# Kernel tuning notes

Hardware: AMD Instinct MI355X
Metric: run time of the kernel (lower is better)

The kernel has to match this reference:

```python
import jax, jax.numpy as jnp
import numpy as np

B, S, D = 32, 256, 128
K = 16          # num_sample (negatives + the positive appended last)
V = 50000       # vocab / num_classes


def setup_inputs() -> dict:
    key = jax.random.key(0)
    k1, k2, k3, k4 = jax.random.split(key, 4)
    return {
        "input_latent": jax.random.normal(k1, (B, S, D), dtype=jnp.float32),
        "target_labels": jax.random.randint(k2, (B, S), 0, V, dtype=jnp.int64),
        "batch_samples": jax.random.randint(k3, (B, S * (K - 1)), 0, V, dtype=jnp.int64),
        "embed_weight": jax.random.normal(k4, (V, D), dtype=jnp.float32),
    }


def reference(input_latent, target_labels, batch_samples, embed_weight):
    b, s, d = input_latent.shape
    out_emb = embed_weight[target_labels]                      # [B,S,D] positives
    neg_emb = embed_weight[batch_samples].reshape(b, s, K - 1, d)
    # Candidates per target position j: K-1 negatives + the positive itself (last)
    samples = jnp.concatenate([neg_emb, out_emb[:, :, None, :]], axis=2)  # [B,S,K,D]
    # sample_rep[b,i,j,k] = latent[b,i] . samples[b,j,k]
    sample_scores = jnp.einsum('bid,bjkd->bijk', input_latent, samples)   # [B,S,S,K]
    # output_rep[b,i,j] = latent[b,i] . out_emb[b,j] (== sample_scores[...,K-1])
    out_scores = jnp.einsum('bid,bjd->bij', input_latent, out_emb)        # [B,S,S]
    # log( exp(out - max) / sum_k exp(sample - max) ) = out - logsumexp(sample)
    lse = jax.scipy.special.logsumexp(sample_scores, axis=3)              # [B,S,S]
    return out_scores - lse
```

## Files before the change

kernel.cpp:

```cpp
#include <hip/hip_runtime.h>
#include <hip/hip_bf16.h>
#include <math.h>

#define BB 32
#define SS 256
#define DD 128
#define KK 16
#define VV 50000
#define SK (SS*KK)
#define LOG2E 1.44269504f
#define LN2   0.69314718f

typedef __attribute__((ext_vector_type(8))) short bf16x8;
typedef __attribute__((ext_vector_type(4))) float f32x4;
typedef __attribute__((ext_vector_type(16))) float f32x16;
typedef unsigned short ushort_t;

static __device__ __forceinline__ short f2bf(float f) {
    __hip_bfloat16 h = __float2bfloat16(f);
    return *(short*)&h;
}

static __device__ __forceinline__ float fast_exp2(float x) {
    float r; asm("v_exp_f32 %0, %1" : "=v"(r) : "v"(x)); return r;
}
static __device__ __forceinline__ float fast_log2(float x) {
    float r; asm("v_log_f32 %0, %1" : "=v"(r) : "v"(x)); return r;
}

static __device__ __forceinline__ int lds_off(int row, int d) {
    return row * 256 + ((d * 2) ^ ((row & 15) << 4));
}

static __device__ __forceinline__ void gload_lds16(const void* g, void* lds) {
    __builtin_amdgcn_global_load_lds(
        (const __attribute__((address_space(1))) unsigned int*)g,
        (__attribute__((address_space(3))) unsigned int*)lds, 16, 0, 0);
}

#define NLAT (BB*SS*DD)
#define NCHUNK_LAT (NLAT/8)

__global__ __launch_bounds__(256)
void convert_lat_kernel(const float* __restrict__ latent,
                        ushort_t* __restrict__ ws_lat)
{
    int i = blockIdx.x * 256 + threadIdx.x;
    if (i >= NCHUNK_LAT) return;
    const float* src = latent + (size_t)i * 8;
    float f[8];
    *(f32x4*)(f + 0) = ((const f32x4*)src)[0];
    *(f32x4*)(f + 4) = ((const f32x4*)src)[1];
    short o[8];
    #pragma unroll
    for (int e = 0; e < 8; ++e) o[e] = f2bf(f[e] * LOG2E);
    *(bf16x8*)(ws_lat + (size_t)i * 8) = *(bf16x8*)o;
}

__global__ __launch_bounds__(256, 2)
void neg_loss_persist(const ushort_t* __restrict__ lat_bf,
                      const int*   __restrict__ labels,
                      const int*   __restrict__ samples,
                      const float* __restrict__ embed,
                      float* __restrict__ out)
{
    __shared__ char  ldsA[SS * 256];
    __shared__ float trans[256][9];

    const int p     = blockIdx.x;
    const int b     = p >> 4;
    const int npair = p & 15;
    const int tid   = threadIdx.x;
    const int wave  = tid >> 6;
    const int lane  = tid & 63;
    const int q     = lane & 15;
    const int sub   = lane >> 4;
    const int l31   = lane & 31;
    const int hi    = lane >> 5;

    const int rB  = wave * 32 + l31;
    const int gc0 = (npair * 2) * 128 + rB;
    const int gc1 = gc0 + 128;
    const int j0i = gc0 >> 4, k0i = gc0 & 15;
    const int j1i = gc1 >> 4, k1i = gc1 & 15;
    const int idx0 = (k0i < 15)
        ? samples[(size_t)b * (SS * (KK - 1)) + j0i * (KK - 1) + k0i]
        : labels[b * SS + j0i];
    const int idx1 = (k1i < 15)
        ? samples[(size_t)b * (SS * (KK - 1)) + j1i * (KK - 1) + k1i]
        : labels[b * SS + j1i];

    f32x4 fbA[16];
    {
        const float* rowp = embed + (size_t)idx0 * DD + hi * 8;
        #pragma unroll
        for (int ks = 0; ks < 8; ++ks) {
            fbA[2 * ks]     = *(const f32x4*)(rowp + ks * 16);
            fbA[2 * ks + 1] = *(const f32x4*)(rowp + ks * 16 + 4);
        }
    }

    #pragma unroll
    for (int t = 0; t < 16; ++t) {
        const int r0 = wave * 64 + t * 4;
        const int r  = r0 + sub;
        const ushort_t* src = lat_bf + ((size_t)(b * SS + r) * DD)
                                     + ((q ^ (r & 15)) << 3);
        gload_lds16(src, ldsA + r0 * 256);
    }

    __syncthreads();

    f32x4 fbB[16];
    {
        const float* rowp = embed + (size_t)idx1 * DD + hi * 8;
        #pragma unroll
        for (int ks = 0; ks < 8; ++ks) {
            fbB[2 * ks]     = *(const f32x4*)(rowp + ks * 16);
            fbB[2 * ks + 1] = *(const f32x4*)(rowp + ks * 16 + 4);
        }
    }

    #pragma unroll
    for (int t = 0; t < 2; ++t) {
        const int tile_n = npair * 2 + t;
        const int jc     = wave * 2 + hi;

        bf16x8 av[8];
        #pragma unroll
        for (int ks = 0; ks < 8; ++ks) {
            const f32x4 lo  = t ? fbB[2 * ks]     : fbA[2 * ks];
            const f32x4 hi4 = t ? fbB[2 * ks + 1] : fbA[2 * ks + 1];
            short t8[8];
            #pragma unroll
            for (int e = 0; e < 4; ++e) t8[e]     = f2bf(lo[e]);
            #pragma unroll
            for (int e = 0; e < 4; ++e) t8[4 + e] = f2bf(hi4[e]);
            av[ks] = *(bf16x8*)t8;
        }

        f32x16 acc[4][2] = {};
        #pragma unroll
        for (int ks = 0; ks < 8; ++ks) {
            const int d = ks * 16 + hi * 8;
            #pragma unroll
            for (int mt = 0; mt < 4; ++mt) {
                bf16x8 bv0 = *(const bf16x8*)(ldsA + lds_off(mt * 64 + l31, d));
                bf16x8 bv1 = *(const bf16x8*)(ldsA + lds_off(mt * 64 + 32 + l31, d));
                acc[mt][0] = __builtin_amdgcn_mfma_f32_32x32x16_bf16(av[ks], bv0, acc[mt][0], 0, 0, 0);
                acc[mt][1] = __builtin_amdgcn_mfma_f32_32x32x16_bf16(av[ks], bv1, acc[mt][1], 0, 0, 0);
            }
        }

        #pragma unroll
        for (int mt = 0; mt < 4; ++mt) {
            #pragma unroll
            for (int f = 0; f < 2; ++f) {
                const f32x16 v = acc[mt][f];
                float pm0 = fmaxf(fmaxf(fmaxf(v[0], v[1]), fmaxf(v[2], v[3])),
                                  fmaxf(fmaxf(v[4], v[5]), fmaxf(v[6], v[7])));
                float pm1 = fmaxf(fmaxf(fmaxf(v[8], v[9]), fmaxf(v[10], v[11])),
                                  fmaxf(fmaxf(v[12], v[13]), fmaxf(v[14], v[15])));
                float om0 = fmaxf(pm0, __shfl_xor(pm0, 32));
                float om1 = fmaxf(pm1, __shfl_xor(pm1, 32));
                float e0 = ((fast_exp2(v[0] - om0) + fast_exp2(v[1] - om0))
                          + (fast_exp2(v[2] - om0) + fast_exp2(v[3] - om0)))
                         + ((fast_exp2(v[4] - om0) + fast_exp2(v[5] - om0))
                          + (fast_exp2(v[6] - om0) + fast_exp2(v[7] - om0)));
                float e1 = ((fast_exp2(v[8]  - om1) + fast_exp2(v[9]  - om1))
                          + (fast_exp2(v[10] - om1) + fast_exp2(v[11] - om1)))
                         + ((fast_exp2(v[12] - om1) + fast_exp2(v[13] - om1))
                          + (fast_exp2(v[14] - om1) + fast_exp2(v[15] - om1)));
                float s0 = e0 + __shfl_xor(e0, 32);
                float s1 = e1 + __shfl_xor(e1, 32);
                float pos0 = __shfl_xor(v[7], 32);
                float pos1 = v[15];
                const float pos = hi ? pos1 : pos0;
                const float om  = hi ? om1  : om0;
                const float s   = hi ? s1   : s0;
                const int i = mt * 64 + f * 32 + l31;
                trans[i][jc] = (pos - om - fast_log2(s)) * LN2;
            }
        }

        __syncthreads();

        {
            const int i = tid;
            float r[8];
            #pragma unroll
            for (int c = 0; c < 8; ++c) r[c] = trans[i][c];
            float* dst = out + ((size_t)b * SS + i) * SS + tile_n * 8;
            *(f32x4*)(dst)     = *(f32x4*)(r);
            *(f32x4*)(dst + 4) = *(f32x4*)(r + 4);
        }

        if (t == 0) __syncthreads();
    }
}

__global__ __launch_bounds__(256, 2)
void neg_loss_fused(const float* __restrict__ latent,
                    const int*   __restrict__ labels,
                    const int*   __restrict__ samples,
                    const float* __restrict__ embed,
                    float* __restrict__ out)
{
    __shared__ char  ldsA[SS * 256];
    __shared__ float trans[256][9];

    const int p     = blockIdx.x;
    const int b     = p >> 4;
    const int npair = p & 15;
    const int tid   = threadIdx.x;
    const int wave  = tid >> 6;
    const int lane  = tid & 63;
    const int l31   = lane & 31;
    const int hi    = lane >> 5;

    const int rB  = wave * 32 + l31;
    const int gc0 = (npair * 2) * 128 + rB;
    const int gc1 = gc0 + 128;
    const int j0i = gc0 >> 4, k0i = gc0 & 15;
    const int j1i = gc1 >> 4, k1i = gc1 & 15;
    const int idx0 = (k0i < 15)
        ? samples[(size_t)b * (SS * (KK - 1)) + j0i * (KK - 1) + k0i]
        : labels[b * SS + j0i];
    const int idx1 = (k1i < 15)
        ? samples[(size_t)b * (SS * (KK - 1)) + j1i * (KK - 1) + k1i]
        : labels[b * SS + j1i];

    f32x4 fbA[16];
    {
        const float* rowp = embed + (size_t)idx0 * DD + hi * 8;
        #pragma unroll
        for (int ks = 0; ks < 8; ++ks) {
            fbA[2 * ks]     = *(const f32x4*)(rowp + ks * 16);
            fbA[2 * ks + 1] = *(const f32x4*)(rowp + ks * 16 + 4);
        }
    }

    #pragma unroll
    for (int pr = 0; pr < 4; ++pr) {
        const int r  = pr * 64 + (tid >> 2);
        const int d0 = (tid & 3) * 32;
        const float* src = latent + ((size_t)b * SS + r) * DD + d0;
        f32x4 f[8];
        #pragma unroll
        for (int c = 0; c < 8; ++c) f[c] = *(const f32x4*)(src + 4 * c);
        short o[32];
        #pragma unroll
        for (int c = 0; c < 8; ++c)
            #pragma unroll
            for (int e = 0; e < 4; ++e)
                o[4 * c + e] = f2bf(f[c][e] * LOG2E);
        #pragma unroll
        for (int c = 0; c < 4; ++c)
            *(bf16x8*)(ldsA + lds_off(r, d0 + 8 * c)) = *(bf16x8*)(o + 8 * c);
    }

    __syncthreads();

    f32x4 fbB[16];
    {
        const float* rowp = embed + (size_t)idx1 * DD + hi * 8;
        #pragma unroll
        for (int ks = 0; ks < 8; ++ks) {
            fbB[2 * ks]     = *(const f32x4*)(rowp + ks * 16);
            fbB[2 * ks + 1] = *(const f32x4*)(rowp + ks * 16 + 4);
        }
    }

    #pragma unroll
    for (int t = 0; t < 2; ++t) {
        const int tile_n = npair * 2 + t;
        const int jc     = wave * 2 + hi;

        bf16x8 av[8];
        #pragma unroll
        for (int ks = 0; ks < 8; ++ks) {
            const f32x4 lo  = t ? fbB[2 * ks]     : fbA[2 * ks];
            const f32x4 hi4 = t ? fbB[2 * ks + 1] : fbA[2 * ks + 1];
            short t8[8];
            #pragma unroll
            for (int e = 0; e < 4; ++e) t8[e]     = f2bf(lo[e]);
            #pragma unroll
            for (int e = 0; e < 4; ++e) t8[4 + e] = f2bf(hi4[e]);
            av[ks] = *(bf16x8*)t8;
        }

        f32x16 acc[4][2] = {};
        #pragma unroll
        for (int ks = 0; ks < 8; ++ks) {
            const int d = ks * 16 + hi * 8;
            #pragma unroll
            for (int mt = 0; mt < 4; ++mt) {
                bf16x8 bv0 = *(const bf16x8*)(ldsA + lds_off(mt * 64 + l31, d));
                bf16x8 bv1 = *(const bf16x8*)(ldsA + lds_off(mt * 64 + 32 + l31, d));
                acc[mt][0] = __builtin_amdgcn_mfma_f32_32x32x16_bf16(av[ks], bv0, acc[mt][0], 0, 0, 0);
                acc[mt][1] = __builtin_amdgcn_mfma_f32_32x32x16_bf16(av[ks], bv1, acc[mt][1], 0, 0, 0);
            }
        }

        #pragma unroll
        for (int mt = 0; mt < 4; ++mt) {
            #pragma unroll
            for (int f = 0; f < 2; ++f) {
                const f32x16 v = acc[mt][f];
                float pm0 = fmaxf(fmaxf(fmaxf(v[0], v[1]), fmaxf(v[2], v[3])),
                                  fmaxf(fmaxf(v[4], v[5]), fmaxf(v[6], v[7])));
                float pm1 = fmaxf(fmaxf(fmaxf(v[8], v[9]), fmaxf(v[10], v[11])),
                                  fmaxf(fmaxf(v[12], v[13]), fmaxf(v[14], v[15])));
                float om0 = fmaxf(pm0, __shfl_xor(pm0, 32));
                float om1 = fmaxf(pm1, __shfl_xor(pm1, 32));
                float e0 = ((fast_exp2(v[0] - om0) + fast_exp2(v[1] - om0))
                          + (fast_exp2(v[2] - om0) + fast_exp2(v[3] - om0)))
                         + ((fast_exp2(v[4] - om0) + fast_exp2(v[5] - om0))
                          + (fast_exp2(v[6] - om0) + fast_exp2(v[7] - om0)));
                float e1 = ((fast_exp2(v[8]  - om1) + fast_exp2(v[9]  - om1))
                          + (fast_exp2(v[10] - om1) + fast_exp2(v[11] - om1)))
                         + ((fast_exp2(v[12] - om1) + fast_exp2(v[13] - om1))
                          + (fast_exp2(v[14] - om1) + fast_exp2(v[15] - om1)));
                float s0 = e0 + __shfl_xor(e0, 32);
                float s1 = e1 + __shfl_xor(e1, 32);
                float pos0 = __shfl_xor(v[7], 32);
                float pos1 = v[15];
                const float pos = hi ? pos1 : pos0;
                const float om  = hi ? om1  : om0;
                const float s   = hi ? s1   : s0;
                const int i = mt * 64 + f * 32 + l31;
                trans[i][jc] = (pos - om - fast_log2(s)) * LN2;
            }
        }

        __syncthreads();

        {
            const int i = tid;
            float r[8];
            #pragma unroll
            for (int c = 0; c < 8; ++c) r[c] = trans[i][c];
            float* dst = out + ((size_t)b * SS + i) * SS + tile_n * 8;
            *(f32x4*)(dst)     = *(f32x4*)(r);
            *(f32x4*)(dst + 4) = *(f32x4*)(r + 4);
        }

        if (t == 0) __syncthreads();
    }
}

extern "C" void kernel_launch(void* const* d_in, const int* in_sizes, int n_in,
                              void* d_out, int out_size, void* d_ws, size_t ws_size,
                              hipStream_t stream) {
    const float* latent  = (const float*)d_in[0];
    const int*   labels  = (const int*)d_in[1];
    const int*   samples = (const int*)d_in[2];
    const float* embed   = (const float*)d_in[3];
    float* out = (float*)d_out;

    if (ws_size >= (size_t)NLAT * 2) {
        ushort_t* ws_lat = (ushort_t*)d_ws;
        convert_lat_kernel<<<(NCHUNK_LAT + 255) / 256, 256, 0, stream>>>(
            latent, ws_lat);
        neg_loss_persist<<<dim3(512), dim3(256), 0, stream>>>(
            ws_lat, labels, samples, embed, out);
    } else {
        neg_loss_fused<<<dim3(512), dim3(256), 0, stream>>>(
            latent, labels, samples, embed, out);
    }
}
```

Measured before the change: 32.36 us.

## Replace persistent kernel with 128-column tiles and LDS-staged coalesced embedding gather

The main kernel now launches a 32x32 grid where each block handles 128 candidate columns instead of 256. It gathers embedding rows coalesced, with lanes sharing indices via shuffle so one row is read by 32 lanes of float4, then stages them as bf16 in LDS. The latent half-tiles are loaded into LDS in two passes of 128 rows, which halves LDS use. Results are written straight to global memory without the LDS transpose, so the stores become strided 4-byte writes. This trades more blocks and less LDS for better gather coalescing and occupancy, at the risk of uncoalesced output stores.

```diff
diff --git a/kernel.cpp b/kernel.cpp
--- a/kernel.cpp
+++ b/kernel.cpp
@@ -12,6 +12,7 @@
 #define LN2   0.69314718f
 
 typedef __attribute__((ext_vector_type(8))) short bf16x8;
+typedef __attribute__((ext_vector_type(4))) short bf16x4;
 typedef __attribute__((ext_vector_type(4))) float f32x4;
 typedef __attribute__((ext_vector_type(16))) float f32x16;
 typedef unsigned short ushort_t;
@@ -58,11 +59,134 @@
 }
 
 __global__ __launch_bounds__(256, 2)
-void neg_loss_persist(const ushort_t* __restrict__ lat_bf,
-                      const int*   __restrict__ labels,
-                      const int*   __restrict__ samples,
-                      const float* __restrict__ embed,
-                      float* __restrict__ out)
+void neg_loss_main(const ushort_t* __restrict__ lat_bf,
+                   const int*   __restrict__ labels,
+                   const int*   __restrict__ samples,
+                   const float* __restrict__ embed,
+                   float* __restrict__ out)
+{
+    __shared__ char ldsA[128 * 256];
+    __shared__ char ldsB[128 * 256];
+
+    const int nt   = blockIdx.x;
+    const int b    = blockIdx.y;
+    const int n0   = nt * 128;
+    const int tid  = threadIdx.x;
+    const int wave = tid >> 6;
+    const int lane = tid & 63;
+    const int q    = lane & 15;
+    const int sub  = lane >> 4;
+    const int l31  = lane & 31;
+    const int hi   = lane >> 5;
+
+    const int gc  = n0 + wave * 32 + l31;
+    const int j   = gc >> 4;
+    const int k   = gc & 15;
+    const int idx_mine = (k < 15)
+        ? samples[(size_t)b * (SS * (KK - 1)) + j * (KK - 1) + k]
+        : labels[b * SS + j];
+
+    f32x4 fb[16];
+    #pragma unroll
+    for (int t = 0; t < 16; ++t) {
+        const int idx_t = __shfl(idx_mine, 2 * t + hi);
+        fb[t] = *(const f32x4*)(embed + (size_t)idx_t * DD + l31 * 4);
+    }
+
+    #pragma unroll
+    for (int t = 0; t < 8; ++t) {
+        const int r0 = wave * 32 + t * 4;
+        const int r  = r0 + sub;
+        const ushort_t* src = lat_bf + ((size_t)(b * SS + r) * DD)
+                                     + ((q ^ (r & 15)) << 3);
+        gload_lds16(src, ldsA + r0 * 256);
+    }
+
+    #pragma unroll
+    for (int t = 0; t < 16; ++t) {
+        const int row = wave * 32 + 2 * t + hi;
+        short o[4];
+        #pragma unroll
+        for (int e = 0; e < 4; ++e) o[e] = f2bf(fb[t][e]);
+        *(bf16x4*)(ldsB + row * 256 + ((l31 * 8) ^ ((row & 15) << 4)))
+            = *(bf16x4*)o;
+    }
+
+    __syncthreads();
+
+    const int jcol = nt * 8 + wave * 2 + hi;
+
+    #pragma unroll
+    for (int mh = 0; mh < 2; ++mh) {
+        if (mh == 1) {
+            __syncthreads();
+            #pragma unroll
+            for (int t = 0; t < 8; ++t) {
+                const int r0 = wave * 32 + t * 4;
+                const int r  = r0 + sub;
+                const ushort_t* src = lat_bf
+                    + ((size_t)(b * SS + 128 + r) * DD)
+                    + ((q ^ (r & 15)) << 3);
+                gload_lds16(src, ldsA + r0 * 256);
+            }
+            __syncthreads();
+        }
+
+        const int rB = wave * 32 + l31;
+        f32x16 acc[2][2] = {};
+        #pragma unroll
+        for (int ks = 0; ks < 8; ++ks) {
+            const int d = ks * 16 + hi * 8;
+            bf16x8 av = *(const bf16x8*)(ldsB + lds_off(rB, d));
+            #pragma unroll
+            for (int mt = 0; mt < 2; ++mt) {
+                bf16x8 bv0 = *(const bf16x8*)(ldsA + lds_off(mt * 64 + l31, d));
+                bf16x8 bv1 = *(const bf16x8*)(ldsA + lds_off(mt * 64 + 32 + l31, d));
+                acc[mt][0] = __builtin_amdgcn_mfma_f32_32x32x16_bf16(av, bv0, acc[mt][0], 0, 0, 0);
+                acc[mt][1] = __builtin_amdgcn_mfma_f32_32x32x16_bf16(av, bv1, acc[mt][1], 0, 0, 0);
+            }
+        }
+
+        #pragma unroll
+        for (int mt = 0; mt < 2; ++mt) {
+            #pragma unroll
+            for (int f = 0; f < 2; ++f) {
+                const f32x16 v = acc[mt][f];
+                float pm0 = fmaxf(fmaxf(fmaxf(v[0], v[1]), fmaxf(v[2], v[3])),
+                                  fmaxf(fmaxf(v[4], v[5]), fmaxf(v[6], v[7])));
+                float pm1 = fmaxf(fmaxf(fmaxf(v[8], v[9]), fmaxf(v[10], v[11])),
+                                  fmaxf(fmaxf(v[12], v[13]), fmaxf(v[14], v[15])));
+                float om0 = fmaxf(pm0, __shfl_xor(pm0, 32));
+                float om1 = fmaxf(pm1, __shfl_xor(pm1, 32));
+                float e0 = ((fast_exp2(v[0] - om0) + fast_exp2(v[1] - om0))
+                          + (fast_exp2(v[2] - om0) + fast_exp2(v[3] - om0)))
+                         + ((fast_exp2(v[4] - om0) + fast_exp2(v[5] - om0))
+                          + (fast_exp2(v[6] - om0) + fast_exp2(v[7] - om0)));
+                float e1 = ((fast_exp2(v[8]  - om1) + fast_exp2(v[9]  - om1))
+                          + (fast_exp2(v[10] - om1) + fast_exp2(v[11] - om1)))
+                         + ((fast_exp2(v[12] - om1) + fast_exp2(v[13] - om1))
+                          + (fast_exp2(v[14] - om1) + fast_exp2(v[15] - om1)));
+                float s0 = e0 + __shfl_xor(e0, 32);
+                float s1 = e1 + __shfl_xor(e1, 32);
+                float pos0 = __shfl_xor(v[7], 32);
+                float pos1 = v[15];
+                const float pos = hi ? pos1 : pos0;
+                const float om  = hi ? om1  : om0;
+                const float s   = hi ? s1   : s0;
+                const int i = mh * 128 + mt * 64 + f * 32 + l31;
+                out[((size_t)b * SS + i) * SS + jcol]
+                    = (pos - om - fast_log2(s)) * LN2;
+            }
+        }
+    }
+}
+
+__global__ __launch_bounds__(256, 2)
+void neg_loss_fused(const float* __restrict__ latent,
+                    const int*   __restrict__ labels,
+                    const int*   __restrict__ samples,
+                    const float* __restrict__ embed,
+                    float* __restrict__ out)
 {
     __shared__ char  ldsA[SS * 256];
     __shared__ float trans[256][9];
@@ -73,8 +197,6 @@
     const int tid   = threadIdx.x;
     const int wave  = tid >> 6;
     const int lane  = tid & 63;
-    const int q     = lane & 15;
-    const int sub   = lane >> 4;
     const int l31   = lane & 31;
     const int hi    = lane >> 5;
 
@@ -101,12 +223,22 @@
     }
 
     #pragma unroll
-    for (int t = 0; t < 16; ++t) {
-        const int r0 = wave * 64 + t * 4;
-        const int r  = r0 + sub;
-        const ushort_t* src = lat_bf + ((size_t)(b * SS + r) * DD)
-                                     + ((q ^ (r & 15)) << 3);
-        gload_lds16(src, ldsA + r0 * 256);
+    for (int pr = 0; pr < 4; ++pr) {
+        const int r  = pr * 64 + (tid >> 2);
+        const int d0 = (tid & 3) * 32;
+        const float* src = latent + ((size_t)b * SS + r) * DD + d0;
+        f32x4 f[8];
+        #pragma unroll
+        for (int c = 0; c < 8; ++c) f[c] = *(const f32x4*)(src + 4 * c);
+        short o[32];
+        #pragma unroll
+        for (int c = 0; c < 8; ++c)
+            #pragma unroll
+            for (int e = 0; e < 4; ++e)
+                o[4 * c + e] = f2bf(f[c][e] * LOG2E);
+        #pragma unroll
+        for (int c = 0; c < 4; ++c)
+            *(bf16x8*)(ldsA + lds_off(r, d0 + 8 * c)) = *(bf16x8*)(o + 8 * c);
     }
 
     __syncthreads();
@@ -199,156 +331,6 @@
     }
 }
 
-__global__ __launch_bounds__(256, 2)
-void neg_loss_fused(const float* __restrict__ latent,
-                    const int*   __restrict__ labels,
-                    const int*   __restrict__ samples,
-                    const float* __restrict__ embed,
-                    float* __restrict__ out)
-{
-    __shared__ char  ldsA[SS * 256];
-    __shared__ float trans[256][9];
-
-    const int p     = blockIdx.x;
-    const int b     = p >> 4;
-    const int npair = p & 15;
-    const int tid   = threadIdx.x;
-    const int wave  = tid >> 6;
-    const int lane  = tid & 63;
-    const int l31   = lane & 31;
-    const int hi    = lane >> 5;
-
-    const int rB  = wave * 32 + l31;
-    const int gc0 = (npair * 2) * 128 + rB;
-    const int gc1 = gc0 + 128;
-    const int j0i = gc0 >> 4, k0i = gc0 & 15;
-    const int j1i = gc1 >> 4, k1i = gc1 & 15;
-    const int idx0 = (k0i < 15)
-        ? samples[(size_t)b * (SS * (KK - 1)) + j0i * (KK - 1) + k0i]
-        : labels[b * SS + j0i];
-    const int idx1 = (k1i < 15)
-        ? samples[(size_t)b * (SS * (KK - 1)) + j1i * (KK - 1) + k1i]
-        : labels[b * SS + j1i];
-
-    f32x4 fbA[16];
-    {
-        const float* rowp = embed + (size_t)idx0 * DD + hi * 8;
-        #pragma unroll
-        for (int ks = 0; ks < 8; ++ks) {
-            fbA[2 * ks]     = *(const f32x4*)(rowp + ks * 16);
-            fbA[2 * ks + 1] = *(const f32x4*)(rowp + ks * 16 + 4);
-        }
-    }
-
-    #pragma unroll
-    for (int pr = 0; pr < 4; ++pr) {
-        const int r  = pr * 64 + (tid >> 2);
-        const int d0 = (tid & 3) * 32;
-        const float* src = latent + ((size_t)b * SS + r) * DD + d0;
-        f32x4 f[8];
-        #pragma unroll
-        for (int c = 0; c < 8; ++c) f[c] = *(const f32x4*)(src + 4 * c);
-        short o[32];
-        #pragma unroll
-        for (int c = 0; c < 8; ++c)
-            #pragma unroll
-            for (int e = 0; e < 4; ++e)
-                o[4 * c + e] = f2bf(f[c][e] * LOG2E);
-        #pragma unroll
-        for (int c = 0; c < 4; ++c)
-            *(bf16x8*)(ldsA + lds_off(r, d0 + 8 * c)) = *(bf16x8*)(o + 8 * c);
-    }
-
-    __syncthreads();
-
-    f32x4 fbB[16];
-    {
-        const float* rowp = embed + (size_t)idx1 * DD + hi * 8;
-        #pragma unroll
-        for (int ks = 0; ks < 8; ++ks) {
-            fbB[2 * ks]     = *(const f32x4*)(rowp + ks * 16);
-            fbB[2 * ks + 1] = *(const f32x4*)(rowp + ks * 16 + 4);
-        }
-    }
-
-    #pragma unroll
-    for (int t = 0; t < 2; ++t) {
-        const int tile_n = npair * 2 + t;
-        const int jc     = wave * 2 + hi;
-
-        bf16x8 av[8];
-        #pragma unroll
-        for (int ks = 0; ks < 8; ++ks) {
-            const f32x4 lo  = t ? fbB[2 * ks]     : fbA[2 * ks];
-            const f32x4 hi4 = t ? fbB[2 * ks + 1] : fbA[2 * ks + 1];
-            short t8[8];
-            #pragma unroll
-            for (int e = 0; e < 4; ++e) t8[e]     = f2bf(lo[e]);
-            #pragma unroll
-            for (int e = 0; e < 4; ++e) t8[4 + e] = f2bf(hi4[e]);
-            av[ks] = *(bf16x8*)t8;
-        }
-
-        f32x16 acc[4][2] = {};
-        #pragma unroll
-        for (int ks = 0; ks < 8; ++ks) {
-            const int d = ks * 16 + hi * 8;
-            #pragma unroll
-            for (int mt = 0; mt < 4; ++mt) {
-                bf16x8 bv0 = *(const bf16x8*)(ldsA + lds_off(mt * 64 + l31, d));
-                bf16x8 bv1 = *(const bf16x8*)(ldsA + lds_off(mt * 64 + 32 + l31, d));
-                acc[mt][0] = __builtin_amdgcn_mfma_f32_32x32x16_bf16(av[ks], bv0, acc[mt][0], 0, 0, 0);
-                acc[mt][1] = __builtin_amdgcn_mfma_f32_32x32x16_bf16(av[ks], bv1, acc[mt][1], 0, 0, 0);
-            }
-        }
-
-        #pragma unroll
-        for (int mt = 0; mt < 4; ++mt) {
-            #pragma unroll
-            for (int f = 0; f < 2; ++f) {
-                const f32x16 v = acc[mt][f];
-                float pm0 = fmaxf(fmaxf(fmaxf(v[0], v[1]), fmaxf(v[2], v[3])),
-                                  fmaxf(fmaxf(v[4], v[5]), fmaxf(v[6], v[7])));
-                float pm1 = fmaxf(fmaxf(fmaxf(v[8], v[9]), fmaxf(v[10], v[11])),
-                                  fmaxf(fmaxf(v[12], v[13]), fmaxf(v[14], v[15])));
-                float om0 = fmaxf(pm0, __shfl_xor(pm0, 32));
-                float om1 = fmaxf(pm1, __shfl_xor(pm1, 32));
-                float e0 = ((fast_exp2(v[0] - om0) + fast_exp2(v[1] - om0))
-                          + (fast_exp2(v[2] - om0) + fast_exp2(v[3] - om0)))
-                         + ((fast_exp2(v[4] - om0) + fast_exp2(v[5] - om0))
-                          + (fast_exp2(v[6] - om0) + fast_exp2(v[7] - om0)));
-                float e1 = ((fast_exp2(v[8]  - om1) + fast_exp2(v[9]  - om1))
-                          + (fast_exp2(v[10] - om1) + fast_exp2(v[11] - om1)))
-                         + ((fast_exp2(v[12] - om1) + fast_exp2(v[13] - om1))
-                          + (fast_exp2(v[14] - om1) + fast_exp2(v[15] - om1)));
-                float s0 = e0 + __shfl_xor(e0, 32);
-                float s1 = e1 + __shfl_xor(e1, 32);
-                float pos0 = __shfl_xor(v[7], 32);
-                float pos1 = v[15];
-                const float pos = hi ? pos1 : pos0;
-                const float om  = hi ? om1  : om0;
-                const float s   = hi ? s1   : s0;
-                const int i = mt * 64 + f * 32 + l31;
-                trans[i][jc] = (pos - om - fast_log2(s)) * LN2;
-            }
-        }
-
-        __syncthreads();
-
-        {
-            const int i = tid;
-            float r[8];
-            #pragma unroll
-            for (int c = 0; c < 8; ++c) r[c] = trans[i][c];
-            float* dst = out + ((size_t)b * SS + i) * SS + tile_n * 8;
-            *(f32x4*)(dst)     = *(f32x4*)(r);
-            *(f32x4*)(dst + 4) = *(f32x4*)(r + 4);
-        }
-
-        if (t == 0) __syncthreads();
-    }
-}
-
 extern "C" void kernel_launch(void* const* d_in, const int* in_sizes, int n_in,
                               void* d_out, int out_size, void* d_ws, size_t ws_size,
                               hipStream_t stream) {
@@ -362,7 +344,7 @@
         ushort_t* ws_lat = (ushort_t*)d_ws;
         convert_lat_kernel<<<(NCHUNK_LAT + 255) / 256, 256, 0, stream>>>(
             latent, ws_lat);
-        neg_loss_persist<<<dim3(512), dim3(256), 0, stream>>>(
+        neg_loss_main<<<dim3(32, 32), dim3(256), 0, stream>>>(
             ws_lat, labels, samples, embed, out);
     } else {
         neg_loss_fused<<<dim3(512), dim3(256), 0, stream>>>(
```

After: 35.05 us. 1.08x slower.

## Write outputs directly from registers, hoist second embed gather, add MFMA priority

Applied to the files above, without the earlier changes.

Drops the LDS transpose buffer and its barriers, so each lane stores its scalar result straight to global memory instead of staging through shared memory for 32-byte vector stores. The second embedding-row gather is issued together with the first, before the latent LDS load, to overlap more memory latency. The MFMA loop is wrapped in s_setprio to favour matrix issue. In exchange, output stores become scattered 4-byte writes with poor coalescing, and holding both gathered rows live raises register pressure.

```diff
diff --git a/kernel.cpp b/kernel.cpp
--- a/kernel.cpp
+++ b/kernel.cpp
@@ -64,8 +64,7 @@
                       const float* __restrict__ embed,
                       float* __restrict__ out)
 {
-    __shared__ char  ldsA[SS * 256];
-    __shared__ float trans[256][9];
+    __shared__ char ldsA[SS * 256];
 
     const int p     = blockIdx.x;
     const int b     = p >> 4;
@@ -90,13 +89,19 @@
         ? samples[(size_t)b * (SS * (KK - 1)) + j1i * (KK - 1) + k1i]
         : labels[b * SS + j1i];
 
-    f32x4 fbA[16];
+    f32x4 fbA[16], fbB[16];
     {
-        const float* rowp = embed + (size_t)idx0 * DD + hi * 8;
-        #pragma unroll
-        for (int ks = 0; ks < 8; ++ks) {
-            fbA[2 * ks]     = *(const f32x4*)(rowp + ks * 16);
-            fbA[2 * ks + 1] = *(const f32x4*)(rowp + ks * 16 + 4);
+        const float* rowp0 = embed + (size_t)idx0 * DD + hi * 8;
+        const float* rowp1 = embed + (size_t)idx1 * DD + hi * 8;
+        #pragma unroll
+        for (int ks = 0; ks < 8; ++ks) {
+            fbA[2 * ks]     = *(const f32x4*)(rowp0 + ks * 16);
+            fbA[2 * ks + 1] = *(const f32x4*)(rowp0 + ks * 16 + 4);
+        }
+        #pragma unroll
+        for (int ks = 0; ks < 8; ++ks) {
+            fbB[2 * ks]     = *(const f32x4*)(rowp1 + ks * 16);
+            fbB[2 * ks + 1] = *(const f32x4*)(rowp1 + ks * 16 + 4);
         }
     }
 
@@ -111,20 +116,9 @@
 
     __syncthreads();
 
-    f32x4 fbB[16];
-    {
-        const float* rowp = embed + (size_t)idx1 * DD + hi * 8;
-        #pragma unroll
-        for (int ks = 0; ks < 8; ++ks) {
-            fbB[2 * ks]     = *(const f32x4*)(rowp + ks * 16);
-            fbB[2 * ks + 1] = *(const f32x4*)(rowp + ks * 16 + 4);
-        }
-    }
-
     #pragma unroll
     for (int t = 0; t < 2; ++t) {
-        const int tile_n = npair * 2 + t;
-        const int jc     = wave * 2 + hi;
+        const int jcol = (npair * 2 + t) * 8 + wave * 2 + hi;
 
         bf16x8 av[8];
         #pragma unroll
@@ -140,6 +134,7 @@
         }
 
         f32x16 acc[4][2] = {};
+        __builtin_amdgcn_s_setprio(1);
         #pragma unroll
         for (int ks = 0; ks < 8; ++ks) {
             const int d = ks * 16 + hi * 8;
@@ -151,6 +146,7 @@
                 acc[mt][1] = __builtin_amdgcn_mfma_f32_32x32x16_bf16(av[ks], bv1, acc[mt][1], 0, 0, 0);
             }
         }
+        __builtin_amdgcn_s_setprio(0);
 
         #pragma unroll
         for (int mt = 0; mt < 4; ++mt) {
@@ -179,23 +175,10 @@
                 const float om  = hi ? om1  : om0;
                 const float s   = hi ? s1   : s0;
                 const int i = mt * 64 + f * 32 + l31;
-                trans[i][jc] = (pos - om - fast_log2(s)) * LN2;
+                out[((size_t)b * SS + i) * SS + jcol]
+                    = (pos - om - fast_log2(s)) * LN2;
             }
         }
-
-        __syncthreads();
-
-        {
-            const int i = tid;
-            float r[8];
-            #pragma unroll
-            for (int c = 0; c < 8; ++c) r[c] = trans[i][c];
-            float* dst = out + ((size_t)b * SS + i) * SS + tile_n * 8;
-            *(f32x4*)(dst)     = *(f32x4*)(r);
-            *(f32x4*)(dst + 4) = *(f32x4*)(r + 4);
-        }
-
-        if (t == 0) __syncthreads();
     }
 }
 
@@ -206,8 +189,7 @@
                     const float* __restrict__ embed,
                     float* __restrict__ out)
 {
-    __shared__ char  ldsA[SS * 256];
-    __shared__ float trans[256][9];
+    __shared__ char ldsA[SS * 256];
 
     const int p     = blockIdx.x;
     const int b     = p >> 4;
@@ -230,13 +212,19 @@
         ? samples[(size_t)b * (SS * (KK - 1)) + j1i * (KK - 1) + k1i]
         : labels[b * SS + j1i];
 
-    f32x4 fbA[16];
+    f32x4 fbA[16], fbB[16];
     {
-        const float* rowp = embed + (size_t)idx0 * DD + hi * 8;
-        #pragma unroll
-        for (int ks = 0; ks < 8; ++ks) {
-            fbA[2 * ks]     = *(const f32x4*)(rowp + ks * 16);
-            fbA[2 * ks + 1] = *(const f32x4*)(rowp + ks * 16 + 4);
+        const float* rowp0 = embed + (size_t)idx0 * DD + hi * 8;
+        const float* rowp1 = embed + (size_t)idx1 * DD + hi * 8;
+        #pragma unroll
+        for (int ks = 0; ks < 8; ++ks) {
+            fbA[2 * ks]     = *(const f32x4*)(rowp0 + ks * 16);
+            fbA[2 * ks + 1] = *(const f32x4*)(rowp0 + ks * 16 + 4);
+        }
+        #pragma unroll
+        for (int ks = 0; ks < 8; ++ks) {
+            fbB[2 * ks]     = *(const f32x4*)(rowp1 + ks * 16);
+            fbB[2 * ks + 1] = *(const f32x4*)(rowp1 + ks * 16 + 4);
         }
     }
 
@@ -261,20 +249,9 @@
 
     __syncthreads();
 
-    f32x4 fbB[16];
-    {
-        const float* rowp = embed + (size_t)idx1 * DD + hi * 8;
-        #pragma unroll
-        for (int ks = 0; ks < 8; ++ks) {
-            fbB[2 * ks]     = *(const f32x4*)(rowp + ks * 16);
-            fbB[2 * ks + 1] = *(const f32x4*)(rowp + ks * 16 + 4);
-        }
-    }
-
     #pragma unroll
     for (int t = 0; t < 2; ++t) {
-        const int tile_n = npair * 2 + t;
-        const int jc     = wave * 2 + hi;
+        const int jcol = (npair * 2 + t) * 8 + wave * 2 + hi;
 
         bf16x8 av[8];
         #pragma unroll
@@ -290,6 +267,7 @@
         }
 
         f32x16 acc[4][2] = {};
+        __builtin_amdgcn_s_setprio(1);
         #pragma unroll
         for (int ks = 0; ks < 8; ++ks) {
             const int d = ks * 16 + hi * 8;
@@ -301,6 +279,7 @@
                 acc[mt][1] = __builtin_amdgcn_mfma_f32_32x32x16_bf16(av[ks], bv1, acc[mt][1], 0, 0, 0);
             }
         }
+        __builtin_amdgcn_s_setprio(0);
 
         #pragma unroll
         for (int mt = 0; mt < 4; ++mt) {
@@ -329,23 +308,10 @@
                 const float om  = hi ? om1  : om0;
                 const float s   = hi ? s1   : s0;
                 const int i = mt * 64 + f * 32 + l31;
-                trans[i][jc] = (pos - om - fast_log2(s)) * LN2;
+                out[((size_t)b * SS + i) * SS + jcol]
+                    = (pos - om - fast_log2(s)) * LN2;
             }
         }
-
-        __syncthreads();
-
-        {
-            const int i = tid;
-            float r[8];
-            #pragma unroll
-            for (int c = 0; c < 8; ++c) r[c] = trans[i][c];
-            float* dst = out + ((size_t)b * SS + i) * SS + tile_n * 8;
-            *(f32x4*)(dst)     = *(f32x4*)(r);
-            *(f32x4*)(dst + 4) = *(f32x4*)(r + 4);
-        }
-
-        if (t == 0) __syncthreads();
     }
 }
 
```

Result: slower. 34.00 us (+5.1%).
